# Performance work log

Hardware: AMD Instinct MI355X
Metric: run time of the kernel (lower is better)

The kernel has to match this reference:

```python
import jax, jax.numpy as jnp
import numpy as np


def setup_inputs() -> dict:
    key = jax.random.key(0)
    k1, k2, k3, k4 = jax.random.split(key, 4)
    N, C, R, G = 524288, 256, 16, 512
    x = jax.random.normal(k1, (N, C), dtype=jnp.float32)
    segment_ids = jnp.sort(jax.random.randint(k2, (N,), 0, G)).astype(jnp.int64)
    # MLP params (Linear stores weight as [out,in] in torch; we keep [in,out] and matmul)
    W1 = jax.random.normal(k3, (C, C // R), dtype=jnp.float32) * (1.0 / np.sqrt(C))
    b1 = jnp.zeros((C // R,), dtype=jnp.float32)
    W2 = jax.random.normal(k4, (C // R, C), dtype=jnp.float32) * (1.0 / np.sqrt(C // R))
    b2 = jnp.zeros((C,), dtype=jnp.float32)
    return {"x": x, "segment_ids": segment_ids, "num_graphs": G,
            "W1": W1, "b1": b1, "W2": W2, "b2": b2}


def reference(x, segment_ids, num_graphs, W1, b1, W2, b2):
    # Per-graph avg pooling: segment sum / node counts. [G, C]
    sums = jax.ops.segment_sum(x, segment_ids, num_segments=num_graphs)
    counts = jax.ops.segment_sum(jnp.ones((x.shape[0],), dtype=x.dtype),
                                 segment_ids, num_segments=num_graphs)
    avg_pool = sums / jnp.maximum(counts, 1.0)[:, None]
    # Per-graph max pooling; guard empty segments (segment_max fills with -inf)
    max_pool = jax.ops.segment_max(x, segment_ids, num_segments=num_graphs)
    max_pool = jnp.where(counts[:, None] > 0, max_pool, 0.0)

    def mlp(p):
        return jax.nn.relu(p @ W1 + b1) @ W2 + b2

    channel_att = jax.nn.sigmoid(mlp(avg_pool) + mlp(max_pool))  # [G, C]
    # Broadcast each graph's attention vector to its nodes (segment gather)
    return x * channel_att[segment_ids]
```

## Files before the change

kernel.cpp:

```cpp
#include <hip/hip_runtime.h>
#include <cfloat>
#include <cmath>

#define CCH 256
#define HID 16

typedef float f32x4 __attribute__((ext_vector_type(4)));

__global__ __launch_bounds__(512) void fused_gca_kernel(
    const float* __restrict__ x, const int* __restrict__ seg,
    const int* __restrict__ numg,
    const float* __restrict__ W1, const float* __restrict__ b1,
    const float* __restrict__ W2, const float* __restrict__ b2,
    float* __restrict__ out, int N)
{
    const int G = *numg;
    const int tid = (int)threadIdx.x;
    const int c4  = tid & 63;
    const int r   = tid >> 6;

    __shared__ f32x4 lsum[512];
    __shared__ f32x4 lmax[512];
    __shared__ float pool2[2 * CCH];
    __shared__ float ht[2 * HID];
    __shared__ float attn[CCH];

    for (int g = (int)blockIdx.x; g < G; g += (int)gridDim.x) {
        int lo = 0, hi = N;
        while (lo < hi) { int mid = (lo + hi) >> 1; if (seg[mid] < g) lo = mid + 1; else hi = mid; }
        const int start = lo;
        hi = N;
        while (lo < hi) { int mid = (lo + hi) >> 1; if (seg[mid] <= g) lo = mid + 1; else hi = mid; }
        const int end = lo;
        const int count = end - start;

        f32x4 s = {0.f, 0.f, 0.f, 0.f};
        f32x4 m = {-FLT_MAX, -FLT_MAX, -FLT_MAX, -FLT_MAX};
        const float* xp = x + (size_t)c4 * 4;
        int n = start + r;
        for (; n + 24 < end; n += 32) {
            const f32x4 v0 = *reinterpret_cast<const f32x4*>(xp + (size_t)(n)      * CCH);
            const f32x4 v1 = *reinterpret_cast<const f32x4*>(xp + (size_t)(n + 8)  * CCH);
            const f32x4 v2 = *reinterpret_cast<const f32x4*>(xp + (size_t)(n + 16) * CCH);
            const f32x4 v3 = *reinterpret_cast<const f32x4*>(xp + (size_t)(n + 24) * CCH);
            s += v0;
            m.x = fmaxf(m.x, v0.x); m.y = fmaxf(m.y, v0.y);
            m.z = fmaxf(m.z, v0.z); m.w = fmaxf(m.w, v0.w);
            s += v1;
            m.x = fmaxf(m.x, v1.x); m.y = fmaxf(m.y, v1.y);
            m.z = fmaxf(m.z, v1.z); m.w = fmaxf(m.w, v1.w);
            s += v2;
            m.x = fmaxf(m.x, v2.x); m.y = fmaxf(m.y, v2.y);
            m.z = fmaxf(m.z, v2.z); m.w = fmaxf(m.w, v2.w);
            s += v3;
            m.x = fmaxf(m.x, v3.x); m.y = fmaxf(m.y, v3.y);
            m.z = fmaxf(m.z, v3.z); m.w = fmaxf(m.w, v3.w);
        }
        for (; n < end; n += 8) {
            const f32x4 v0 = *reinterpret_cast<const f32x4*>(xp + (size_t)n * CCH);
            s += v0;
            m.x = fmaxf(m.x, v0.x); m.y = fmaxf(m.y, v0.y);
            m.z = fmaxf(m.z, v0.z); m.w = fmaxf(m.w, v0.w);
        }
        lsum[tid] = s; lmax[tid] = m;
        __syncthreads();

        if (tid < 64) {
            f32x4 S = lsum[tid];
            f32x4 M = lmax[tid];
            #pragma unroll
            for (int k = 1; k < 8; ++k) {
                const f32x4 S2 = lsum[tid + 64 * k];
                const f32x4 M2 = lmax[tid + 64 * k];
                S += S2;
                M.x = fmaxf(M.x, M2.x); M.y = fmaxf(M.y, M2.y);
                M.z = fmaxf(M.z, M2.z); M.w = fmaxf(M.w, M2.w);
            }
            const float inv = (count > 0) ? 1.0f / (float)count : 0.0f;
            pool2[4 * tid + 0] = S.x * inv;
            pool2[4 * tid + 1] = S.y * inv;
            pool2[4 * tid + 2] = S.z * inv;
            pool2[4 * tid + 3] = S.w * inv;
            pool2[CCH + 4 * tid + 0] = (count > 0) ? M.x : 0.0f;
            pool2[CCH + 4 * tid + 1] = (count > 0) ? M.y : 0.0f;
            pool2[CCH + 4 * tid + 2] = (count > 0) ? M.z : 0.0f;
            pool2[CCH + 4 * tid + 3] = (count > 0) ? M.w : 0.0f;
        }
        __syncthreads();

        {
            const int pair = tid >> 4;
            const int sub  = tid & 15;
            const int j    = pair & (HID - 1);
            const float* p = pool2 + (pair >> 4) * CCH;
            float h = 0.f;
            #pragma unroll
            for (int c = sub; c < CCH; c += 16)
                h = fmaf(p[c], W1[c * HID + j], h);
            h += __shfl_xor(h, 8, 64);
            h += __shfl_xor(h, 4, 64);
            h += __shfl_xor(h, 2, 64);
            h += __shfl_xor(h, 1, 64);
            if (sub == 0) ht[pair] = fmaxf(h + b1[j], 0.0f);
        }
        __syncthreads();

        if (tid < CCH) {
            float acc = 2.0f * b2[tid];
            #pragma unroll
            for (int j = 0; j < HID; ++j)
                acc = fmaf(ht[j] + ht[HID + j], W2[j * CCH + tid], acc);
            attn[tid] = 1.0f / (1.0f + expf(-acc));
        }
        __syncthreads();

        {
            const f32x4 a4 = *reinterpret_cast<const f32x4*>(attn + c4 * 4);
            const int rem = end - (start + r);
            if (rem > 0) {
                const int rows = (rem + 7) >> 3;
                int k = rows - 1;
                const float* xq = x   + (size_t)(start + r) * CCH + (size_t)c4 * 4;
                float*       oq = out + (size_t)(start + r) * CCH + (size_t)c4 * 4;
                for (; k >= 3; k -= 4) {
                    const size_t i0 = (size_t)(k)     * (8 * CCH);
                    const size_t i1 = (size_t)(k - 1) * (8 * CCH);
                    const size_t i2 = (size_t)(k - 2) * (8 * CCH);
                    const size_t i3 = (size_t)(k - 3) * (8 * CCH);
                    const f32x4 v0 = *reinterpret_cast<const f32x4*>(xq + i0);
                    const f32x4 v1 = *reinterpret_cast<const f32x4*>(xq + i1);
                    const f32x4 v2 = *reinterpret_cast<const f32x4*>(xq + i2);
                    const f32x4 v3 = *reinterpret_cast<const f32x4*>(xq + i3);
                    __builtin_nontemporal_store(v0 * a4, reinterpret_cast<f32x4*>(oq + i0));
                    __builtin_nontemporal_store(v1 * a4, reinterpret_cast<f32x4*>(oq + i1));
                    __builtin_nontemporal_store(v2 * a4, reinterpret_cast<f32x4*>(oq + i2));
                    __builtin_nontemporal_store(v3 * a4, reinterpret_cast<f32x4*>(oq + i3));
                }
                for (; k >= 0; --k) {
                    const size_t i0 = (size_t)k * (8 * CCH);
                    const f32x4 v0 = *reinterpret_cast<const f32x4*>(xq + i0);
                    __builtin_nontemporal_store(v0 * a4, reinterpret_cast<f32x4*>(oq + i0));
                }
            }
        }
        __syncthreads();
    }
}

extern "C" void kernel_launch(void* const* d_in, const int* in_sizes, int n_in,
                              void* d_out, int out_size, void* d_ws, size_t ws_size,
                              hipStream_t stream) {
    const float* x    = (const float*)d_in[0];
    const int*   seg  = (const int*)d_in[1];
    const int*   numg = (const int*)d_in[2];
    const float* W1   = (const float*)d_in[3];
    const float* b1   = (const float*)d_in[4];
    const float* W2   = (const float*)d_in[5];
    const float* b2   = (const float*)d_in[6];
    float* out = (float*)d_out;

    const int N = in_sizes[1];

    fused_gca_kernel<<<512, 512, 0, stream>>>(x, seg, numg, W1, b1, W2, b2, out, N);
}
```

Measured before the change: 291.9 us.

## Split fused kernel into pool+MLP kernel and separate attention-apply kernel

```diff
diff --git a/kernel.cpp b/kernel.cpp
--- a/kernel.cpp
+++ b/kernel.cpp
@@ -7,23 +7,22 @@
 
 typedef float f32x4 __attribute__((ext_vector_type(4)));
 
-__global__ __launch_bounds__(512) void fused_gca_kernel(
+__global__ __launch_bounds__(1024, 8) void pool_mlp_kernel(
     const float* __restrict__ x, const int* __restrict__ seg,
     const int* __restrict__ numg,
     const float* __restrict__ W1, const float* __restrict__ b1,
     const float* __restrict__ W2, const float* __restrict__ b2,
-    float* __restrict__ out, int N)
+    float* __restrict__ att, int N)
 {
     const int G = *numg;
     const int tid = (int)threadIdx.x;
     const int c4  = tid & 63;
     const int r   = tid >> 6;
 
-    __shared__ f32x4 lsum[512];
-    __shared__ f32x4 lmax[512];
+    __shared__ f32x4 lsum[1024];
+    __shared__ f32x4 lmax[1024];
     __shared__ float pool2[2 * CCH];
     __shared__ float ht[2 * HID];
-    __shared__ float attn[CCH];
 
     for (int g = (int)blockIdx.x; g < G; g += (int)gridDim.x) {
         int lo = 0, hi = N;
@@ -38,25 +37,17 @@
         f32x4 m = {-FLT_MAX, -FLT_MAX, -FLT_MAX, -FLT_MAX};
         const float* xp = x + (size_t)c4 * 4;
         int n = start + r;
-        for (; n + 24 < end; n += 32) {
+        for (; n + 16 < end; n += 32) {
             const f32x4 v0 = *reinterpret_cast<const f32x4*>(xp + (size_t)(n)      * CCH);
-            const f32x4 v1 = *reinterpret_cast<const f32x4*>(xp + (size_t)(n + 8)  * CCH);
-            const f32x4 v2 = *reinterpret_cast<const f32x4*>(xp + (size_t)(n + 16) * CCH);
-            const f32x4 v3 = *reinterpret_cast<const f32x4*>(xp + (size_t)(n + 24) * CCH);
+            const f32x4 v1 = *reinterpret_cast<const f32x4*>(xp + (size_t)(n + 16) * CCH);
             s += v0;
             m.x = fmaxf(m.x, v0.x); m.y = fmaxf(m.y, v0.y);
             m.z = fmaxf(m.z, v0.z); m.w = fmaxf(m.w, v0.w);
             s += v1;
             m.x = fmaxf(m.x, v1.x); m.y = fmaxf(m.y, v1.y);
             m.z = fmaxf(m.z, v1.z); m.w = fmaxf(m.w, v1.w);
-            s += v2;
-            m.x = fmaxf(m.x, v2.x); m.y = fmaxf(m.y, v2.y);
-            m.z = fmaxf(m.z, v2.z); m.w = fmaxf(m.w, v2.w);
-            s += v3;
-            m.x = fmaxf(m.x, v3.x); m.y = fmaxf(m.y, v3.y);
-            m.z = fmaxf(m.z, v3.z); m.w = fmaxf(m.w, v3.w);
         }
-        for (; n < end; n += 8) {
+        if (n < end) {
             const f32x4 v0 = *reinterpret_cast<const f32x4*>(xp + (size_t)n * CCH);
             s += v0;
             m.x = fmaxf(m.x, v0.x); m.y = fmaxf(m.y, v0.y);
@@ -69,7 +60,7 @@
             f32x4 S = lsum[tid];
             f32x4 M = lmax[tid];
             #pragma unroll
-            for (int k = 1; k < 8; ++k) {
+            for (int k = 1; k < 16; ++k) {
                 const f32x4 S2 = lsum[tid + 64 * k];
                 const f32x4 M2 = lmax[tid + 64 * k];
                 S += S2;
@@ -88,7 +79,7 @@
         }
         __syncthreads();
 
-        {
+        if (tid < 512) {
             const int pair = tid >> 4;
             const int sub  = tid & 15;
             const int j    = pair & (HID - 1);
@@ -110,40 +101,52 @@
             #pragma unroll
             for (int j = 0; j < HID; ++j)
                 acc = fmaf(ht[j] + ht[HID + j], W2[j * CCH + tid], acc);
-            attn[tid] = 1.0f / (1.0f + expf(-acc));
+            att[(size_t)g * CCH + tid] = 1.0f / (1.0f + expf(-acc));
         }
         __syncthreads();
+    }
+}
 
-        {
-            const f32x4 a4 = *reinterpret_cast<const f32x4*>(attn + c4 * 4);
-            const int rem = end - (start + r);
-            if (rem > 0) {
-                const int rows = (rem + 7) >> 3;
-                int k = rows - 1;
-                const float* xq = x   + (size_t)(start + r) * CCH + (size_t)c4 * 4;
-                float*       oq = out + (size_t)(start + r) * CCH + (size_t)c4 * 4;
-                for (; k >= 3; k -= 4) {
-                    const size_t i0 = (size_t)(k)     * (8 * CCH);
-                    const size_t i1 = (size_t)(k - 1) * (8 * CCH);
-                    const size_t i2 = (size_t)(k - 2) * (8 * CCH);
-                    const size_t i3 = (size_t)(k - 3) * (8 * CCH);
-                    const f32x4 v0 = *reinterpret_cast<const f32x4*>(xq + i0);
-                    const f32x4 v1 = *reinterpret_cast<const f32x4*>(xq + i1);
-                    const f32x4 v2 = *reinterpret_cast<const f32x4*>(xq + i2);
-                    const f32x4 v3 = *reinterpret_cast<const f32x4*>(xq + i3);
-                    __builtin_nontemporal_store(v0 * a4, reinterpret_cast<f32x4*>(oq + i0));
-                    __builtin_nontemporal_store(v1 * a4, reinterpret_cast<f32x4*>(oq + i1));
-                    __builtin_nontemporal_store(v2 * a4, reinterpret_cast<f32x4*>(oq + i2));
-                    __builtin_nontemporal_store(v3 * a4, reinterpret_cast<f32x4*>(oq + i3));
-                }
-                for (; k >= 0; --k) {
-                    const size_t i0 = (size_t)k * (8 * CCH);
-                    const f32x4 v0 = *reinterpret_cast<const f32x4*>(xq + i0);
-                    __builtin_nontemporal_store(v0 * a4, reinterpret_cast<f32x4*>(oq + i0));
-                }
-            }
+__global__ __launch_bounds__(512, 8) void apply_att_kernel(
+    const float* __restrict__ x, const int* __restrict__ seg,
+    const int* __restrict__ numg,
+    const float* __restrict__ att, float* __restrict__ out, int N)
+{
+    const int G = *numg;
+    const int tid = (int)threadIdx.x;
+    const int c4  = tid & 63;
+    const int r   = tid >> 6;
+
+    for (int gg = (int)blockIdx.x; gg < 2 * G; gg += (int)gridDim.x) {
+        const int g  = gg >> 1;
+        const int vw = (r << 1) | (gg & 1);
+
+        int lo = 0, hi = N;
+        while (lo < hi) { int mid = (lo + hi) >> 1; if (seg[mid] < g) lo = mid + 1; else hi = mid; }
+        const int start = lo;
+        hi = N;
+        while (lo < hi) { int mid = (lo + hi) >> 1; if (seg[mid] <= g) lo = mid + 1; else hi = mid; }
+        const int end = lo;
+
+        const f32x4 a4 = *reinterpret_cast<const f32x4*>(att + (size_t)g * CCH + c4 * 4);
+
+        const int rem = end - (start + vw);
+        if (rem <= 0) continue;
+        int k = ((rem + 15) >> 4) - 1;
+        const float* xq = x   + (size_t)(start + vw) * CCH + (size_t)c4 * 4;
+        float*       oq = out + (size_t)(start + vw) * CCH + (size_t)c4 * 4;
+        for (; k >= 1; k -= 2) {
+            const size_t i0 = (size_t)(k)     * (16 * CCH);
+            const size_t i1 = (size_t)(k - 1) * (16 * CCH);
+            const f32x4 v0 = *reinterpret_cast<const f32x4*>(xq + i0);
+            const f32x4 v1 = *reinterpret_cast<const f32x4*>(xq + i1);
+            __builtin_nontemporal_store(v0 * a4, reinterpret_cast<f32x4*>(oq + i0));
+            __builtin_nontemporal_store(v1 * a4, reinterpret_cast<f32x4*>(oq + i1));
         }
-        __syncthreads();
+        if (k == 0) {
+            const f32x4 v0 = *reinterpret_cast<const f32x4*>(xq);
+            __builtin_nontemporal_store(v0 * a4, reinterpret_cast<f32x4*>(oq));
+        }
     }
 }
 
@@ -158,8 +161,10 @@
     const float* W2   = (const float*)d_in[5];
     const float* b2   = (const float*)d_in[6];
     float* out = (float*)d_out;
+    float* att = (float*)d_ws;
 
     const int N = in_sizes[1];
 
-    fused_gca_kernel<<<512, 512, 0, stream>>>(x, seg, numg, W1, b1, W2, b2, out, N);
+    pool_mlp_kernel<<<512, 1024, 0, stream>>>(x, seg, numg, W1, b1, W2, b2, att, N);
+    apply_att_kernel<<<1024, 512, 0, stream>>>(x, seg, numg, att, out, N);
 }
```

Result: slower. 371.6 us (+27.3%).
